# Kernel tuning notes

Hardware: AMD Instinct MI355X
Metric: run time of the kernel (lower is better)

## Reference

```python
import jax, jax.numpy as jnp
import numpy as np

DIM, NH, HD = 512, 16, 32          # dim, num_heads, head_dim
WH, WW = 7, 7                      # window size
N = WH * WW                        # tokens per window = 49
B_ = 2048                          # num_windows * batch


def _relative_position_index():
    # Static integer index table, identical to the torch buffer construction.
    coords = np.stack(np.meshgrid(np.arange(WH), np.arange(WW), indexing='ij'))  # (2,WH,WW)
    cf = coords.reshape(2, -1)                                                   # (2,N)
    rel = cf[:, :, None] - cf[:, None, :]                                        # (2,N,N)
    rel = rel.transpose(1, 2, 0).astype(np.int64)                                # (N,N,2)
    rel[:, :, 0] += WH - 1
    rel[:, :, 1] += WW - 1
    rel[:, :, 0] *= 2 * WW - 1
    return jnp.asarray(rel.sum(-1))                                              # (N,N)

REL_IDX = _relative_position_index()


def setup_inputs() -> dict:
    key = jax.random.key(0)
    ks = jax.random.split(key, 6)
    s = 0.02
    return {
        'x': jax.random.normal(ks[0], (B_, N, DIM), dtype=jnp.float32),
        'qkv_w': jax.random.normal(ks[1], (3 * DIM, DIM), dtype=jnp.float32) * s,
        'qkv_b': jax.random.normal(ks[2], (3 * DIM,), dtype=jnp.float32) * s,
        'proj_w': jax.random.normal(ks[3], (DIM, DIM), dtype=jnp.float32) * s,
        'proj_b': jax.random.normal(ks[4], (DIM,), dtype=jnp.float32) * s,
        'bias_table': jax.random.normal(ks[5], (2 * WH - 1, 2 * WW - 1, NH), dtype=jnp.float32) * s,
    }


def reference(x, qkv_w, qkv_b, proj_w, proj_b, bias_table):
    b, n, c = x.shape
    # fused qkv projection, split per the original reshape(B_,N,nH,hd,3)
    qkv = (x @ qkv_w.T + qkv_b).reshape(b, n, NH, HD, 3)
    qkv = qkv.transpose(0, 2, 1, 3, 4)                 # (B_, nH, N, hd, 3)
    q, k, v = qkv[..., 0], qkv[..., 1], qkv[..., 2]
    # gathered relative position bias: (N,N,nH) -> (1,nH,N,N)
    bias = bias_table.reshape(-1, NH)[REL_IDX].transpose(2, 0, 1)[None]
    scale = 1.0 / np.sqrt(HD).astype(np.float32)
    scores = jnp.einsum('bhqd,bhkd->bhqk', q, k) * scale + bias
    attn = jax.nn.softmax(scores, axis=-1)
    out = jnp.einsum('bhqk,bhkd->bhqd', attn, v)       # (B_, nH, N, hd)
    out = out.transpose(0, 2, 1, 3).reshape(b, n, c)
    return out @ proj_w.T + proj_b
```

## Files before the change

kernel.cpp:

```cpp
#include <hip/hip_runtime.h>


typedef __bf16 bf16x8 __attribute__((ext_vector_type(8)));
typedef float f32x4 __attribute__((ext_vector_type(4)));

#define SCALE_Q 0.17677669529663687f

#define OFF_XS     2365440ull
#define OFF_ATTN   136583168ull
#define WS2        507779072ull
#define WS_R2      105119744ull

__device__ __forceinline__ unsigned short f2bf(float f) {
    unsigned int u = __float_as_uint(f);
    u += 0x7FFFu + ((u >> 16) & 1u);
    return (unsigned short)(u >> 16);
}

__device__ __forceinline__ uint4 pack8(const unsigned short o[8]) {
    uint4 p;
    p.x = (unsigned)o[0] | ((unsigned)o[1] << 16);
    p.y = (unsigned)o[2] | ((unsigned)o[3] << 16);
    p.z = (unsigned)o[4] | ((unsigned)o[5] << 16);
    p.w = (unsigned)o[6] | ((unsigned)o[7] << 16);
    return p;
}

union BU8 { bf16x8 v; unsigned short s[8]; };

#define GLOAD16(g, l) __builtin_amdgcn_global_load_lds( \
    (__attribute__((address_space(1))) void*)(void*)(g), \
    (__attribute__((address_space(3))) void*)(l), 16, 0, 0)

__global__ void prepN_kernel(const float* __restrict__ x,
                             const float* __restrict__ qkv_w,
                             const float* __restrict__ qkv_b,
                             const float* __restrict__ proj_w,
                             const float* __restrict__ bias_table,
                             unsigned short* __restrict__ wqkv_f,
                             unsigned short* __restrict__ wproj_f,
                             float* __restrict__ bias_f,
                             float* __restrict__ qkvb_r,
                             unsigned short* __restrict__ xs) {
    int b = blockIdx.x, t = threadIdx.x;
    if (b < 384) {
        int gid = b * 256 + t;
        int c = gid >> 6, k8 = (gid & 63) * 8;
        int head = c / 96, rem = c - head * 96;
        int which = rem >> 5, d = rem & 31;
        const float* src = qkv_w + (size_t)(head * 96 + d * 3 + which) * 512 + k8;
        unsigned short o[8];
#pragma unroll
        for (int j = 0; j < 8; ++j) o[j] = f2bf(src[j]);
        *(uint4*)(wqkv_f + (size_t)c * 512 + k8) = pack8(o);
    } else if (b < 512) {
        int gid = (b - 384) * 256 + t;
        const float* src = proj_w + (size_t)gid * 8;
        unsigned short o[8];
#pragma unroll
        for (int j = 0; j < 8; ++j) o[j] = f2bf(src[j]);
        *(uint4*)(wproj_f + (size_t)gid * 8) = pack8(o);
    } else if (b < 768) {
        int gid = (b - 512) * 256 + t;
        int j = gid & 63; int i = (gid >> 6) & 63; int h = gid >> 12;
        float v = -1e30f;
        if (i < 49 && j < 49) {
            int ri = i / 7, ci = i % 7, rj = j / 7, cj = j % 7;
            int idx = (ri - rj + 6) * 13 + (ci - cj + 6);
            v = bias_table[idx * 16 + h];
        }
        bias_f[gid] = v;
    } else if (b == 768) {
        for (int c = t; c < 1536; c += 256) {
            int head = c / 96, rem = c - head * 96;
            int which = rem >> 5, d = rem & 31;
            qkvb_r[c] = qkv_b[head * 96 + d * 3 + which];
        }
    } else {
        int gid = (b - 769) * 256 + t;
        int row = gid >> 3, kt = gid & 7;
        int win = row >> 6, tok = row & 63; if (tok > 48) tok = 48;
        int sw = row & 7;
        const float* src = x + ((size_t)win * 49 + tok) * 512 + kt * 64;
        unsigned short* dst = xs + (size_t)row * 512 + kt * 64;
#pragma unroll
        for (int c = 0; c < 8; ++c) {
            int cs = (c ^ sw) * 8;
            float4 a = *(const float4*)(src + cs);
            float4 bb = *(const float4*)(src + cs + 4);
            unsigned short o[8];
            o[0] = f2bf(a.x); o[1] = f2bf(a.y); o[2] = f2bf(a.z); o[3] = f2bf(a.w);
            o[4] = f2bf(bb.x); o[5] = f2bf(bb.y); o[6] = f2bf(bb.z); o[7] = f2bf(bb.w);
            *(uint4*)(dst + c * 8) = pack8(o);
        }
    }
}

__global__ __launch_bounds__(256, 2)
void qkvattn_kernel(const unsigned short* __restrict__ xs,
                    const unsigned short* __restrict__ wqkv_f,
                    const float* __restrict__ qkvb_r,
                    const float* __restrict__ bias_f,
                    unsigned short* __restrict__ attnout) {
    __shared__ __align__(16) char smem[53248];
    char* As = smem;
    char* Bs = smem + 16384;

    int i = blockIdx.x;
    int virt = (i & 7) * 2048 + (i >> 3);
    int mb = virt >> 4, head = virt & 15;
    int m0 = mb * 128;

    const int tid = threadIdx.x;
    const int l = tid & 63;
    const int W = tid >> 6;
    const int lr = l & 15;
    const int lg = l >> 4;

    f32x4 acc[2][6];
    const f32x4 zf = {0.f, 0.f, 0.f, 0.f};
#pragma unroll
    for (int mt = 0; mt < 2; ++mt)
#pragma unroll
        for (int nt = 0; nt < 6; ++nt) acc[mt][nt] = zf;

    int rsub = l >> 3, csub = l & 7;
    int cswz = (csub ^ rsub) * 16;
    int clin = csub * 16;

    const char* bbase = (const char*)wqkv_f + (size_t)head * 96 * 1024;

#pragma unroll 1
    for (int kt = 0; kt < 8; ++kt) {
#pragma unroll
        for (int ii = 0; ii < 4; ++ii) {
            int r = ii * 32 + W * 8 + rsub;
            const char* srcA = (const char*)xs +
                ((size_t)(m0 + r) * 512 + kt * 64) * 2 + clin;
            GLOAD16(srcA, As + ii * 4096 + W * 1024);
        }
#pragma unroll
        for (int jj = 0; jj < 3; ++jj) {
            int r = jj * 32 + W * 8 + rsub;
            const char* srcB = bbase + ((size_t)r * 512 + kt * 64) * 2 + cswz;
            GLOAD16(srcB, Bs + jj * 4096 + W * 1024);
        }
        __syncthreads();
#pragma unroll
        for (int ks = 0; ks < 2; ++ks) {
            bf16x8 af[2], bf[6];
#pragma unroll
            for (int mt = 0; mt < 2; ++mt) {
                int row = W * 32 + mt * 16 + lr;
                af[mt] = *(const bf16x8*)(As + row * 128 +
                    ((ks * 64 + lg * 16) ^ ((row & 7) << 4)));
            }
#pragma unroll
            for (int nt = 0; nt < 6; ++nt) {
                int row = nt * 16 + lr;
                bf[nt] = *(const bf16x8*)(Bs + row * 128 +
                    ((ks * 64 + lg * 16) ^ ((row & 7) << 4)));
            }
#pragma unroll
            for (int mt = 0; mt < 2; ++mt)
#pragma unroll
                for (int nt = 0; nt < 6; ++nt)
                    acc[mt][nt] = __builtin_amdgcn_mfma_f32_16x16x32_bf16(
                        af[mt], bf[nt], acc[mt][nt], 0, 0, 0);
        }
        __syncthreads();
    }

    unsigned short* qkvL = (unsigned short*)(smem + 28672);
    {
        unsigned short* wbuf = qkvL + (W >> 1) * 6144;
        int tokb = (W & 1) * 32 + 4 * lg;
#pragma unroll
        for (int nt = 0; nt < 6; ++nt) {
            const int which = nt >> 1;
            const int d = (nt & 1) * 16 + lr;
            float bias = qkvb_r[head * 96 + which * 32 + d];
            float sc = (which == 0) ? SCALE_Q : 1.0f;
#pragma unroll
            for (int mt = 0; mt < 2; ++mt) {
                int tok0 = tokb + mt * 16;
#pragma unroll
                for (int r = 0; r < 4; ++r) {
                    int tok = tok0 + r;
                    float v = acc[mt][nt][r] + bias;
                    if (which == 2) {
                        int idx = 4096 + d * 64 + (((tok >> 3) ^ (d & 7)) << 3) + (tok & 7);
                        wbuf[idx] = f2bf(v);
                    } else {
                        wbuf[which * 2048 + tok * 32 + d] = f2bf(v * sc);
                    }
                }
            }
        }
    }
    __syncthreads();

    {
        const unsigned short* qa = qkvL + (W >> 1) * 6144;
        char* P = smem + W * 4096;
        int win_g = mb * 2 + (W >> 1);
        unsigned short* ao = attnout + (size_t)win_g * (49 * 512);

        bf16x8 qf[2], kf[4];
#pragma unroll
        for (int qt = 0; qt < 2; ++qt)
            qf[qt] = *(const bf16x8*)(qa + ((W & 1) * 32 + qt * 16 + lr) * 32 + lg * 8);
#pragma unroll
        for (int i2 = 0; i2 < 4; ++i2)
            kf[i2] = *(const bf16x8*)(qa + 2048 + (i2 * 16 + lr) * 32 + lg * 8);

        f32x4 s[4][2];
#pragma unroll
        for (int mt = 0; mt < 4; ++mt)
#pragma unroll
            for (int qt = 0; qt < 2; ++qt)
                s[mt][qt] = __builtin_amdgcn_mfma_f32_16x16x32_bf16(
                    kf[mt], qf[qt], zf, 0, 0, 0);
#pragma unroll
        for (int qt = 0; qt < 2; ++qt) {
            int q = (W & 1) * 32 + qt * 16 + lr;
            const float* bb = bias_f + ((size_t)head * 64 + q) * 64;
#pragma unroll
            for (int mt = 0; mt < 4; ++mt) {
                float4 b4 = *(const float4*)(bb + mt * 16 + lg * 4);
                s[mt][qt][0] += b4.x; s[mt][qt][1] += b4.y;
                s[mt][qt][2] += b4.z; s[mt][qt][3] += b4.w;
            }
        }
#pragma unroll
        for (int qt = 0; qt < 2; ++qt) {
            float m = -1e30f;
#pragma unroll
            for (int mt = 0; mt < 4; ++mt)
#pragma unroll
                for (int r = 0; r < 4; ++r) m = fmaxf(m, s[mt][qt][r]);
            m = fmaxf(m, __shfl_xor(m, 16));
            m = fmaxf(m, __shfl_xor(m, 32));
            float sum = 0.f;
#pragma unroll
            for (int mt = 0; mt < 4; ++mt)
#pragma unroll
                for (int r = 0; r < 4; ++r) {
                    float p = __expf(s[mt][qt][r] - m);
                    s[mt][qt][r] = p; sum += p;
                }
            sum += __shfl_xor(sum, 16);
            sum += __shfl_xor(sum, 32);
            float inv = 1.0f / sum;
            int ql = qt * 16 + lr;
            int sw = (ql & 7) << 4;
#pragma unroll
            for (int mt = 0; mt < 4; ++mt) {
                uint2 uv;
                uv.x = (unsigned)f2bf(s[mt][qt][0] * inv) |
                       ((unsigned)f2bf(s[mt][qt][1] * inv) << 16);
                uv.y = (unsigned)f2bf(s[mt][qt][2] * inv) |
                       ((unsigned)f2bf(s[mt][qt][3] * inv) << 16);
                *(uint2*)(P + ql * 128 + ((mt * 32 + lg * 8) ^ sw)) = uv;
            }
        }
        bf16x8 vf[2][2];
#pragma unroll
        for (int ks = 0; ks < 2; ++ks)
#pragma unroll
            for (int nt = 0; nt < 2; ++nt) {
                int d = nt * 16 + lr;
                vf[ks][nt] = *(const bf16x8*)(qa + 4096 + d * 64 +
                    (((ks * 4 + lg) ^ (d & 7)) << 3));
            }
        f32x4 o[2][2];
#pragma unroll
        for (int mt = 0; mt < 2; ++mt) {
            o[mt][0] = zf; o[mt][1] = zf;
            int ql = mt * 16 + lr;
            int sw = (ql & 7) << 4;
#pragma unroll
            for (int ks = 0; ks < 2; ++ks) {
                bf16x8 pf = *(const bf16x8*)(P + ql * 128 + ((ks * 64 + lg * 16) ^ sw));
                o[mt][0] = __builtin_amdgcn_mfma_f32_16x16x32_bf16(pf, vf[ks][0], o[mt][0], 0, 0, 0);
                o[mt][1] = __builtin_amdgcn_mfma_f32_16x16x32_bf16(pf, vf[ks][1], o[mt][1], 0, 0, 0);
            }
        }
#pragma unroll
        for (int mt = 0; mt < 2; ++mt)
#pragma unroll
            for (int nt = 0; nt < 2; ++nt)
#pragma unroll
                for (int r = 0; r < 4; ++r) {
                    int q = (W & 1) * 32 + mt * 16 + 4 * lg + r;
                    if (q < 49)
                        ao[q * 512 + head * 32 + nt * 16 + lr] = f2bf(o[mt][nt][r]);
                }
    }
}

__global__ __launch_bounds__(256, 2)
void proj_kernel(const unsigned short* __restrict__ attnout,
                 const unsigned short* __restrict__ wproj_f,
                 const float* __restrict__ proj_b,
                 float* __restrict__ out) {
    __shared__ __align__(16) char smem[32768];
    char* As = smem;
    char* Bs = smem + 16384;

    int bid = blockIdx.x;
    int c = bid >> 2;
    int cs = (c & 7) * 98 + (c >> 3);
    int m0 = cs * 128;
    int n0 = (bid & 3) * 128;

    const int tid = threadIdx.x;
    const int l = tid & 63;
    const int W = tid >> 6;
    const int lr = l & 15;
    const int lg = l >> 4;
    const int Wm = W >> 1, Wn = W & 1;

    f32x4 acc[4][4];
    const f32x4 zf = {0.f, 0.f, 0.f, 0.f};
#pragma unroll
    for (int mt = 0; mt < 4; ++mt)
#pragma unroll
        for (int nt = 0; nt < 4; ++nt) acc[mt][nt] = zf;

    int rsub = l >> 3;
    int csub = l & 7;
    int cswz = (csub ^ rsub) * 16;

#pragma unroll 1
    for (int kt = 0; kt < 8; ++kt) {
#pragma unroll
        for (int i = 0; i < 4; ++i) {
            int r = i * 32 + W * 8 + rsub;
            const char* srcA = (const char*)attnout +
                ((size_t)(m0 + r) * 512 + kt * 64) * 2 + cswz;
            GLOAD16(srcA, As + i * 4096 + W * 1024);
            const char* srcB = (const char*)wproj_f +
                ((size_t)(n0 + r) * 512 + kt * 64) * 2 + cswz;
            GLOAD16(srcB, Bs + i * 4096 + W * 1024);
        }
        __syncthreads();
#pragma unroll
        for (int ks = 0; ks < 2; ++ks) {
            bf16x8 af[4], bf[4];
#pragma unroll
            for (int mt = 0; mt < 4; ++mt) {
                int row = Wm * 64 + mt * 16 + lr;
                af[mt] = *(const bf16x8*)(As + row * 128 +
                    ((ks * 64 + lg * 16) ^ ((row & 7) << 4)));
            }
#pragma unroll
            for (int nt = 0; nt < 4; ++nt) {
                int row = Wn * 64 + nt * 16 + lr;
                bf[nt] = *(const bf16x8*)(Bs + row * 128 +
                    ((ks * 64 + lg * 16) ^ ((row & 7) << 4)));
            }
#pragma unroll
            for (int mt = 0; mt < 4; ++mt)
#pragma unroll
                for (int nt = 0; nt < 4; ++nt)
                    acc[mt][nt] = __builtin_amdgcn_mfma_f32_16x16x32_bf16(
                        af[mt], bf[nt], acc[mt][nt], 0, 0, 0);
        }
        __syncthreads();
    }
#pragma unroll
    for (int nt = 0; nt < 4; ++nt) {
        int n = n0 + Wn * 64 + nt * 16 + lr;
        float pb = proj_b[n];
#pragma unroll
        for (int mt = 0; mt < 4; ++mt) {
#pragma unroll
            for (int r = 0; r < 4; ++r) {
                int m = m0 + Wm * 64 + mt * 16 + 4 * lg + r;
                out[(size_t)m * 512 + n] = acc[mt][nt][r] + pb;
            }
        }
    }
}

__global__ void prep2_kernel(const float* __restrict__ qkv_w,
                             const float* __restrict__ proj_w,
                             const float* __restrict__ bias_table,
                             unsigned short* __restrict__ wqkv_f,
                             unsigned short* __restrict__ wproj_f,
                             float* __restrict__ bias_f) {
    int b = blockIdx.x, t = threadIdx.x;
    if (b < 384) {
        int gid = b * 256 + t;
        int l = gid & 63; int r = gid >> 6;
        int dh = r & 1; r >>= 1;
        int ks = r & 15; r >>= 4;
        int h = r & 15; int which = r >> 4;
        int d = dh * 16 + (l & 15);
        int row = h * 96 + d * 3 + which;
        int c0 = ks * 32 + (l >> 4) * 8;
        const float* src = qkv_w + row * 512 + c0;
        unsigned short o[8];
#pragma unroll
        for (int j = 0; j < 8; ++j) o[j] = f2bf(src[j]);
        *(uint4*)(wqkv_f + (size_t)gid * 8) = pack8(o);
    } else if (b < 512) {
        int gid = (b - 384) * 256 + t;
        const float* src = proj_w + (size_t)gid * 8;
        unsigned short o[8];
#pragma unroll
        for (int j = 0; j < 8; ++j) o[j] = f2bf(src[j]);
        *(uint4*)(wproj_f + (size_t)gid * 8) = pack8(o);
    } else {
        int gid = (b - 512) * 256 + t;
        int j = gid & 63; int i = (gid >> 6) & 63; int h = gid >> 12;
        float v = -1e30f;
        if (i < 49 && j < 49) {
            int ri = i / 7, ci = i % 7, rj = j / 7, cj = j % 7;
            int idx = (ri - rj + 6) * 13 + (ci - cj + 6);
            v = bias_table[idx * 16 + h];
        }
        bias_f[gid] = v;
    }
}

__global__ __launch_bounds__(256, 2)
void attn_qkv_kernel(const float* __restrict__ x,
                     const float* __restrict__ qkv_b,
                     const unsigned short* __restrict__ wqkv_f,
                     const float* __restrict__ bias_f,
                     unsigned short* __restrict__ attnout) {
    __shared__ __align__(16) char smem[81920];
    const int tid = threadIdx.x;
    const int l = tid & 63;
    const int W = tid >> 6;
    const int lr = l & 15;
    const int lg = l >> 4;
    const int win = blockIdx.x;

    bf16x8 xf[16];
    {
        int trow = 16 * W + lr; if (trow > 48) trow = 48;
        const float* xr = x + ((size_t)win * 49 + trow) * 512;
#pragma unroll
        for (int ks = 0; ks < 16; ++ks) {
            float4 a = *(const float4*)(xr + ks * 32 + lg * 8);
            float4 b = *(const float4*)(xr + ks * 32 + lg * 8 + 4);
            BU8 u;
            u.s[0] = f2bf(a.x); u.s[1] = f2bf(a.y); u.s[2] = f2bf(a.z); u.s[3] = f2bf(a.w);
            u.s[4] = f2bf(b.x); u.s[5] = f2bf(b.y); u.s[6] = f2bf(b.z); u.s[7] = f2bf(b.w);
            xf[ks] = u.v;
        }
    }

    const f32x4 zf = {0.f, 0.f, 0.f, 0.f};
    unsigned short* ao = attnout + (size_t)win * (49 * 512);

    for (int hg = 0; hg < 4; ++hg) {
        for (int h2 = 0; h2 < 4; ++h2) {
            int h = hg * 4 + h2;
            char* qk = smem + h2 * 8192;
            char* vt = smem + 32768 + h2 * 4096;
#pragma unroll 1
            for (int which = 0; which < 3; ++which) {
                f32x4 a0 = zf, a1 = zf;
                const unsigned short* bp =
                    wqkv_f + (size_t)(which * 16 + h) * 16384 + l * 8;
#pragma unroll
                for (int ks = 0; ks < 16; ++ks) {
                    bf16x8 b0 = *(const bf16x8*)(bp + ks * 1024);
                    bf16x8 b1 = *(const bf16x8*)(bp + ks * 1024 + 512);
                    a0 = __builtin_amdgcn_mfma_f32_16x16x32_bf16(xf[ks], b0, a0, 0, 0, 0);
                    a1 = __builtin_amdgcn_mfma_f32_16x16x32_bf16(xf[ks], b1, a1, 0, 0, 0);
                }
                float bias0 = qkv_b[h * 96 + lr * 3 + which];
                float bias1 = qkv_b[h * 96 + (16 + lr) * 3 + which];
                if (which == 2) {
                    int d0 = lr, d1 = 16 + lr;
#pragma unroll
                    for (int r = 0; r < 4; ++r) {
                        int t = 16 * W + 4 * lg + r;
                        *(unsigned short*)(vt + d0 * 128 + ((t * 2) ^ ((d0 & 7) << 4))) =
                            f2bf(a0[r] + bias0);
                        *(unsigned short*)(vt + d1 * 128 + ((t * 2) ^ ((d1 & 7) << 4))) =
                            f2bf(a1[r] + bias1);
                    }
                } else {
                    float sc = (which == 0) ? SCALE_Q : 1.0f;
                    int cb = which * 64;
#pragma unroll
                    for (int r = 0; r < 4; ++r) {
                        int t = 16 * W + 4 * lg + r;
                        int sw = (t & 7) << 4;
                        *(unsigned short*)(qk + t * 128 + ((cb + lr * 2) ^ sw)) =
                            f2bf((a0[r] + bias0) * sc);
                        *(unsigned short*)(qk + t * 128 + ((cb + 32 + lr * 2) ^ sw)) =
                            f2bf((a1[r] + bias1) * sc);
                    }
                }
            }
        }
        __syncthreads();
        {
            int h = hg * 4 + W;
            char* qk = smem + W * 8192;
            char* vt = smem + 32768 + W * 4096;
            char* P  = smem + 49152 + W * 8192;

            bf16x8 kf[4], qf[4];
#pragma unroll
            for (int i = 0; i < 4; ++i) {
                int row = i * 16 + lr;
                int sw = (row & 7) << 4;
                qf[i] = *(const bf16x8*)(qk + row * 128 + ((lg * 16) ^ sw));
                kf[i] = *(const bf16x8*)(qk + row * 128 + ((64 + lg * 16) ^ sw));
            }
            f32x4 s[4][4];
#pragma unroll
            for (int mt = 0; mt < 4; ++mt)
#pragma unroll
                for (int qt = 0; qt < 4; ++qt)
                    s[mt][qt] = __builtin_amdgcn_mfma_f32_16x16x32_bf16(
                        kf[mt], qf[qt], zf, 0, 0, 0);
#pragma unroll
            for (int qt = 0; qt < 4; ++qt) {
                int q = qt * 16 + lr;
                const float* bb = bias_f + ((size_t)h * 64 + q) * 64;
#pragma unroll
                for (int mt = 0; mt < 4; ++mt) {
                    float4 b4 = *(const float4*)(bb + mt * 16 + lg * 4);
                    s[mt][qt][0] += b4.x; s[mt][qt][1] += b4.y;
                    s[mt][qt][2] += b4.z; s[mt][qt][3] += b4.w;
                }
            }
#pragma unroll
            for (int qt = 0; qt < 4; ++qt) {
                float m = -1e30f;
#pragma unroll
                for (int mt = 0; mt < 4; ++mt)
#pragma unroll
                    for (int r = 0; r < 4; ++r) m = fmaxf(m, s[mt][qt][r]);
                m = fmaxf(m, __shfl_xor(m, 16));
                m = fmaxf(m, __shfl_xor(m, 32));
                float sum = 0.f;
#pragma unroll
                for (int mt = 0; mt < 4; ++mt)
#pragma unroll
                    for (int r = 0; r < 4; ++r) {
                        float p = __expf(s[mt][qt][r] - m);
                        s[mt][qt][r] = p; sum += p;
                    }
                sum += __shfl_xor(sum, 16);
                sum += __shfl_xor(sum, 32);
                float inv = 1.0f / sum;
                int qrow = qt * 16 + lr;
                int sw = (qrow & 7) << 4;
#pragma unroll
                for (int mt = 0; mt < 4; ++mt) {
                    uint2 uv;
                    uv.x = (unsigned)f2bf(s[mt][qt][0] * inv) |
                           ((unsigned)f2bf(s[mt][qt][1] * inv) << 16);
                    uv.y = (unsigned)f2bf(s[mt][qt][2] * inv) |
                           ((unsigned)f2bf(s[mt][qt][3] * inv) << 16);
                    *(uint2*)(P + qrow * 128 + ((mt * 32 + lg * 8) ^ sw)) = uv;
                }
            }
            bf16x8 vf[2][2];
#pragma unroll
            for (int ks = 0; ks < 2; ++ks)
#pragma unroll
                for (int nt = 0; nt < 2; ++nt) {
                    int d = nt * 16 + lr;
                    vf[ks][nt] = *(const bf16x8*)(vt + d * 128 +
                        ((ks * 64 + lg * 16) ^ ((d & 7) << 4)));
                }
            f32x4 o[4][2];
#pragma unroll
            for (int mt = 0; mt < 4; ++mt) {
                o[mt][0] = zf; o[mt][1] = zf;
                int q = mt * 16 + lr;
                int sw = (q & 7) << 4;
#pragma unroll
                for (int ks = 0; ks < 2; ++ks) {
                    bf16x8 pf = *(const bf16x8*)(P + q * 128 + ((ks * 64 + lg * 16) ^ sw));
                    o[mt][0] = __builtin_amdgcn_mfma_f32_16x16x32_bf16(pf, vf[ks][0], o[mt][0], 0, 0, 0);
                    o[mt][1] = __builtin_amdgcn_mfma_f32_16x16x32_bf16(pf, vf[ks][1], o[mt][1], 0, 0, 0);
                }
            }
#pragma unroll
            for (int mt = 0; mt < 4; ++mt)
#pragma unroll
                for (int nt = 0; nt < 2; ++nt)
#pragma unroll
                    for (int r = 0; r < 4; ++r) {
                        int q = mt * 16 + 4 * lg + r;
                        if (q < 49)
                            ao[q * 512 + h * 32 + nt * 16 + lr] = f2bf(o[mt][nt][r]);
                    }
        }
        __syncthreads();
    }
}

extern "C" void kernel_launch(void* const* d_in, const int* in_sizes, int n_in,
                              void* d_out, int out_size, void* d_ws, size_t ws_size,
                              hipStream_t stream) {
    const float* x          = (const float*)d_in[0];
    const float* qkv_w      = (const float*)d_in[1];
    const float* qkv_b      = (const float*)d_in[2];
    const float* proj_w     = (const float*)d_in[3];
    const float* proj_b     = (const float*)d_in[4];
    const float* bias_table = (const float*)d_in[5];

    unsigned short* wqkv_f  = (unsigned short*)d_ws;
    unsigned short* wproj_f = wqkv_f + 786432;
    float*          bias_f  = (float*)(wproj_f + 262144);

    if (ws_size >= WS2) {
        float* qkvb_r = (float*)((char*)d_ws + 2359296);
        unsigned short* xs      = (unsigned short*)((char*)d_ws + OFF_XS);
        unsigned short* attnout = (unsigned short*)((char*)d_ws + OFF_ATTN);
        hipLaunchKernelGGL(prepN_kernel, dim3(4865), dim3(256), 0, stream,
                           x, qkv_w, qkv_b, proj_w, bias_table,
                           wqkv_f, wproj_f, bias_f, qkvb_r, xs);
        hipLaunchKernelGGL(qkvattn_kernel, dim3(16384), dim3(256), 0, stream,
                           xs, wqkv_f, qkvb_r, bias_f, attnout);
        hipLaunchKernelGGL(proj_kernel, dim3(3136), dim3(256), 0, stream,
                           attnout, wproj_f, proj_b, (float*)d_out);
    } else if (ws_size >= WS_R2) {
        unsigned short* attnout = (unsigned short*)((char*)d_ws + 2359296);
        hipLaunchKernelGGL(prep2_kernel, dim3(768), dim3(256), 0, stream,
                           qkv_w, proj_w, bias_table, wqkv_f, wproj_f, bias_f);
        hipLaunchKernelGGL(attn_qkv_kernel, dim3(2048), dim3(256), 0, stream,
                           x, qkv_b, wqkv_f, bias_f, attnout);
        hipLaunchKernelGGL(proj_kernel, dim3(3136), dim3(256), 0, stream,
                           attnout, wproj_f, proj_b, (float*)d_out);
    }
}
```

Baseline: 530.7 us.

## Double-buffer QKV GEMM tiles and use hardware bf16 conversion

Gives the QKV projection loop two shared-memory buffers so the next K-tile is loaded while MFMAs run on the current one, with one barrier per iteration instead of two. Replaces the software round-to-nearest bf16 conversion with the compiler's native __bf16 cast throughout. It also vectorises the V-tile stores into ushort4 writes. Shared memory grows from 52 to 80 KB, which still allows the declared two blocks per CU on MI355X's 160 KB LDS, but it may reduce occupancy in practice.

```diff
diff --git a/kernel.cpp b/kernel.cpp
--- a/kernel.cpp
+++ b/kernel.cpp
@@ -10,6 +10,19 @@
 #define OFF_ATTN   136583168ull
 #define WS2        507779072ull
 #define WS_R2      105119744ull
+
+__device__ __forceinline__ unsigned short bfc(float f) {
+    union { __bf16 b; unsigned short u; } x; x.b = (__bf16)f; return x.u;
+}
+
+__device__ __forceinline__ uint4 cvt8(const float f[8]) {
+    uint4 p;
+    p.x = (unsigned)bfc(f[0]) | ((unsigned)bfc(f[1]) << 16);
+    p.y = (unsigned)bfc(f[2]) | ((unsigned)bfc(f[3]) << 16);
+    p.z = (unsigned)bfc(f[4]) | ((unsigned)bfc(f[5]) << 16);
+    p.w = (unsigned)bfc(f[6]) | ((unsigned)bfc(f[7]) << 16);
+    return p;
+}
 
 __device__ __forceinline__ unsigned short f2bf(float f) {
     unsigned int u = __float_as_uint(f);
@@ -49,17 +62,17 @@
         int head = c / 96, rem = c - head * 96;
         int which = rem >> 5, d = rem & 31;
         const float* src = qkv_w + (size_t)(head * 96 + d * 3 + which) * 512 + k8;
-        unsigned short o[8];
-#pragma unroll
-        for (int j = 0; j < 8; ++j) o[j] = f2bf(src[j]);
-        *(uint4*)(wqkv_f + (size_t)c * 512 + k8) = pack8(o);
+        float f[8];
+#pragma unroll
+        for (int j = 0; j < 8; ++j) f[j] = src[j];
+        *(uint4*)(wqkv_f + (size_t)c * 512 + k8) = cvt8(f);
     } else if (b < 512) {
         int gid = (b - 384) * 256 + t;
         const float* src = proj_w + (size_t)gid * 8;
-        unsigned short o[8];
-#pragma unroll
-        for (int j = 0; j < 8; ++j) o[j] = f2bf(src[j]);
-        *(uint4*)(wproj_f + (size_t)gid * 8) = pack8(o);
+        float f[8];
+#pragma unroll
+        for (int j = 0; j < 8; ++j) f[j] = src[j];
+        *(uint4*)(wproj_f + (size_t)gid * 8) = cvt8(f);
     } else if (b < 768) {
         int gid = (b - 512) * 256 + t;
         int j = gid & 63; int i = (gid >> 6) & 63; int h = gid >> 12;
@@ -86,12 +99,10 @@
 #pragma unroll
         for (int c = 0; c < 8; ++c) {
             int cs = (c ^ sw) * 8;
-            float4 a = *(const float4*)(src + cs);
-            float4 bb = *(const float4*)(src + cs + 4);
-            unsigned short o[8];
-            o[0] = f2bf(a.x); o[1] = f2bf(a.y); o[2] = f2bf(a.z); o[3] = f2bf(a.w);
-            o[4] = f2bf(bb.x); o[5] = f2bf(bb.y); o[6] = f2bf(bb.z); o[7] = f2bf(bb.w);
-            *(uint4*)(dst + c * 8) = pack8(o);
+            float f[8];
+            *(float4*)&f[0] = *(const float4*)(src + cs);
+            *(float4*)&f[4] = *(const float4*)(src + cs + 4);
+            *(uint4*)(dst + c * 8) = cvt8(f);
         }
     }
 }
@@ -102,9 +113,9 @@
                     const float* __restrict__ qkvb_r,
                     const float* __restrict__ bias_f,
                     unsigned short* __restrict__ attnout) {
-    __shared__ __align__(16) char smem[53248];
+    __shared__ __align__(16) char smem[81920];
     char* As = smem;
-    char* Bs = smem + 16384;
+    char* Bs = smem + 32768;
 
     int i = blockIdx.x;
     int virt = (i & 7) * 2048 + (i >> 3);
@@ -129,36 +140,56 @@
     int clin = csub * 16;
 
     const char* bbase = (const char*)wqkv_f + (size_t)head * 96 * 1024;
+    const char* abase = (const char*)xs + ((size_t)m0 * 512) * 2;
+
+    {
+#pragma unroll
+        for (int ii = 0; ii < 4; ++ii) {
+            int r = ii * 32 + W * 8 + rsub;
+            GLOAD16(abase + (size_t)r * 1024 + clin, As + ii * 4096 + W * 1024);
+        }
+#pragma unroll
+        for (int jj = 0; jj < 3; ++jj) {
+            int r = jj * 32 + W * 8 + rsub;
+            GLOAD16(bbase + (size_t)r * 1024 + cswz, Bs + jj * 4096 + W * 1024);
+        }
+    }
+    asm volatile("s_waitcnt vmcnt(0)" ::: "memory");
+    __builtin_amdgcn_s_barrier();
+    __builtin_amdgcn_sched_barrier(0);
 
 #pragma unroll 1
     for (int kt = 0; kt < 8; ++kt) {
-#pragma unroll
-        for (int ii = 0; ii < 4; ++ii) {
-            int r = ii * 32 + W * 8 + rsub;
-            const char* srcA = (const char*)xs +
-                ((size_t)(m0 + r) * 512 + kt * 64) * 2 + clin;
-            GLOAD16(srcA, As + ii * 4096 + W * 1024);
-        }
-#pragma unroll
-        for (int jj = 0; jj < 3; ++jj) {
-            int r = jj * 32 + W * 8 + rsub;
-            const char* srcB = bbase + ((size_t)r * 512 + kt * 64) * 2 + cswz;
-            GLOAD16(srcB, Bs + jj * 4096 + W * 1024);
-        }
-        __syncthreads();
+        char* Ac = As + (kt & 1) * 16384;
+        char* Bc = Bs + ((kt & 1) ? 12288 : 0);
+        if (kt < 7) {
+            char* An = As + ((kt & 1) ? 0 : 16384);
+            char* Bn = Bs + ((kt & 1) ? 0 : 12288);
+            int ko = (kt + 1) * 128;
+#pragma unroll
+            for (int ii = 0; ii < 4; ++ii) {
+                int r = ii * 32 + W * 8 + rsub;
+                GLOAD16(abase + (size_t)r * 1024 + ko + clin, An + ii * 4096 + W * 1024);
+            }
+#pragma unroll
+            for (int jj = 0; jj < 3; ++jj) {
+                int r = jj * 32 + W * 8 + rsub;
+                GLOAD16(bbase + (size_t)r * 1024 + ko + cswz, Bn + jj * 4096 + W * 1024);
+            }
+        }
 #pragma unroll
         for (int ks = 0; ks < 2; ++ks) {
             bf16x8 af[2], bf[6];
 #pragma unroll
             for (int mt = 0; mt < 2; ++mt) {
                 int row = W * 32 + mt * 16 + lr;
-                af[mt] = *(const bf16x8*)(As + row * 128 +
+                af[mt] = *(const bf16x8*)(Ac + row * 128 +
                     ((ks * 64 + lg * 16) ^ ((row & 7) << 4)));
             }
 #pragma unroll
             for (int nt = 0; nt < 6; ++nt) {
                 int row = nt * 16 + lr;
-                bf[nt] = *(const bf16x8*)(Bs + row * 128 +
+                bf[nt] = *(const bf16x8*)(Bc + row * 128 +
                     ((ks * 64 + lg * 16) ^ ((row & 7) << 4)));
             }
 #pragma unroll
@@ -168,10 +199,12 @@
                     acc[mt][nt] = __builtin_amdgcn_mfma_f32_16x16x32_bf16(
                         af[mt], bf[nt], acc[mt][nt], 0, 0, 0);
         }
-        __syncthreads();
-    }
-
-    unsigned short* qkvL = (unsigned short*)(smem + 28672);
+        asm volatile("s_waitcnt vmcnt(0)" ::: "memory");
+        __builtin_amdgcn_s_barrier();
+        __builtin_amdgcn_sched_barrier(0);
+    }
+
+    unsigned short* qkvL = (unsigned short*)(smem + 57344);
     {
         unsigned short* wbuf = qkvL + (W >> 1) * 6144;
         int tokb = (W & 1) * 32 + 4 * lg;
@@ -184,16 +217,19 @@
 #pragma unroll
             for (int mt = 0; mt < 2; ++mt) {
                 int tok0 = tokb + mt * 16;
-#pragma unroll
-                for (int r = 0; r < 4; ++r) {
-                    int tok = tok0 + r;
-                    float v = acc[mt][nt][r] + bias;
-                    if (which == 2) {
-                        int idx = 4096 + d * 64 + (((tok >> 3) ^ (d & 7)) << 3) + (tok & 7);
-                        wbuf[idx] = f2bf(v);
-                    } else {
-                        wbuf[which * 2048 + tok * 32 + d] = f2bf(v * sc);
-                    }
+                if (which == 2) {
+                    int idx = 4096 + d * 64 + (((tok0 >> 3) ^ (d & 7)) << 3) + (tok0 & 7);
+                    ushort4 u;
+                    u.x = bfc(acc[mt][nt][0] + bias);
+                    u.y = bfc(acc[mt][nt][1] + bias);
+                    u.z = bfc(acc[mt][nt][2] + bias);
+                    u.w = bfc(acc[mt][nt][3] + bias);
+                    *(ushort4*)(wbuf + idx) = u;
+                } else {
+#pragma unroll
+                    for (int r = 0; r < 4; ++r)
+                        wbuf[which * 2048 + (tok0 + r) * 32 + d] =
+                            bfc((acc[mt][nt][r] + bias) * sc);
                 }
             }
         }
@@ -257,10 +293,10 @@
 #pragma unroll
             for (int mt = 0; mt < 4; ++mt) {
                 uint2 uv;
-                uv.x = (unsigned)f2bf(s[mt][qt][0] * inv) |
-                       ((unsigned)f2bf(s[mt][qt][1] * inv) << 16);
-                uv.y = (unsigned)f2bf(s[mt][qt][2] * inv) |
-                       ((unsigned)f2bf(s[mt][qt][3] * inv) << 16);
+                uv.x = (unsigned)bfc(s[mt][qt][0] * inv) |
+                       ((unsigned)bfc(s[mt][qt][1] * inv) << 16);
+                uv.y = (unsigned)bfc(s[mt][qt][2] * inv) |
+                       ((unsigned)bfc(s[mt][qt][3] * inv) << 16);
                 *(uint2*)(P + ql * 128 + ((mt * 32 + lg * 8) ^ sw)) = uv;
             }
         }
@@ -294,7 +330,7 @@
                 for (int r = 0; r < 4; ++r) {
                     int q = (W & 1) * 32 + mt * 16 + 4 * lg + r;
                     if (q < 49)
-                        ao[q * 512 + head * 32 + nt * 16 + lr] = f2bf(o[mt][nt][r]);
+                        ao[q * 512 + head * 32 + nt * 16 + lr] = bfc(o[mt][nt][r]);
                 }
     }
 }
```

After: 595.9 us. 12.3% more time.
